# Kernel optimization log

Measured on AMD Instinct MI355X. Metric: run time of the kernel, lower is better.

## Reference

```python
import jax, jax.numpy as jnp
import numpy as np

N, E = 50000, 800000
H, C_HID = 4, 64  # heads, hidden_units
C_IN, C_OUT = 256, 64
NEG_SLOPE = 0.2
EPS = 1e-16


def gat_conv(x, src, dst, W, att_src, att_dst, bias):
    """PyG GATConv with concat=False (mean over heads) + bias.
    x: [N, F_in], W: [F_in, H*C], att_*: [H, C], bias: [C]."""
    n = x.shape[0]
    h = (x @ W).reshape(n, H, -1)                     # [N, H, C]
    a_src = jnp.sum(h * att_src, axis=-1)             # [N, H]
    a_dst = jnp.sum(h * att_dst, axis=-1)             # [N, H]
    e = jax.nn.leaky_relu(a_src[src] + a_dst[dst], NEG_SLOPE)  # [E, H]
    # segment softmax grouped by destination node
    m = jax.ops.segment_max(e, dst, num_segments=n)   # [N, H]
    e = jnp.exp(e - m[dst])
    denom = jax.ops.segment_sum(e, dst, num_segments=n)
    alpha = e / (denom[dst] + EPS)                    # [E, H]
    msg = h[src] * alpha[:, :, None]                  # [E, H, C]
    out = jax.ops.segment_sum(msg, dst, num_segments=n)  # [N, H, C]
    return out.mean(axis=1) + bias                    # concat=False -> head mean


def setup_inputs() -> dict:
    key = jax.random.key(0)
    ks = jax.random.split(key, 16)
    inp = {
        "x": jax.random.normal(ks[0], (N, C_IN), dtype=jnp.float32),
        "edge_index": jax.random.randint(ks[1], (2, E), 0, N, dtype=jnp.int64),
    }
    dims = [(C_IN, C_HID), (C_HID, C_HID), (C_HID, C_OUT)]
    for i, (fi, fo) in enumerate(dims, start=1):
        inp[f"W{i}"] = jax.random.normal(ks[2 + 4 * (i - 1)], (fi, H * fo), dtype=jnp.float32) * (1.0 / np.sqrt(fi))
        inp[f"as{i}"] = jax.random.normal(ks[3 + 4 * (i - 1)], (H, fo), dtype=jnp.float32) * 0.1
        inp[f"ad{i}"] = jax.random.normal(ks[4 + 4 * (i - 1)], (H, fo), dtype=jnp.float32) * 0.1
        inp[f"b{i}"] = jnp.zeros((fo,), dtype=jnp.float32)
    return inp


def reference(x, edge_index, W1, as1, ad1, b1, W2, as2, ad2, b2, W3, as3, ad3, b3):
    n = x.shape[0]
    loop = jnp.arange(n, dtype=edge_index.dtype)
    src = jnp.concatenate([edge_index[0], loop])  # add_self_loops=True (PyG default)
    dst = jnp.concatenate([edge_index[1], loop])
    layers = [(W1, as1, ad1, b1), (W2, as2, ad2, b2), (W3, as3, ad3, b3)]
    for (W, a_s, a_d, b) in layers:
        x = gat_conv(x, src, dst, W, a_s, a_d, b)
        x = jax.nn.relu(x)  # dropout is identity at inference
    return jax.nn.log_softmax(x, axis=-1)
```

## Files before the change

### kernel.cpp

```cpp
#include <hip/hip_runtime.h>
#include <hip/hip_bf16.h>
#include <math.h>
#include <stdint.h>

#define HEADS 4
#define CH 64
#define HC 256
#define NEG 0.2f
#define EPSV 1e-16f
#define NEGBIG -3.0e38f

typedef __attribute__((ext_vector_type(8))) short short8;
typedef __attribute__((ext_vector_type(4))) float f32x4;
typedef _Float16 f16_t;
typedef __fp16 fp16x2 __attribute__((ext_vector_type(2)));

__device__ __forceinline__ float lrelu(float x) { return x > 0.f ? x : NEG * x; }

__device__ __forceinline__ unsigned short f2bf(float f) {
  __hip_bfloat16 b = __float2bfloat16(f);
  return *reinterpret_cast<unsigned short*>(&b);
}
__device__ __forceinline__ unsigned short f16b(float f) {
  return __builtin_bit_cast(unsigned short, (f16_t)f);
}
__device__ __forceinline__ float dot2acc(unsigned int a, unsigned int h, float acc) {
#if __has_builtin(__builtin_amdgcn_fdot2)
  return __builtin_amdgcn_fdot2(__builtin_bit_cast(fp16x2, a),
                                __builtin_bit_cast(fp16x2, h), acc, false);
#else
  fp16x2 av = __builtin_bit_cast(fp16x2, a);
  fp16x2 hv = __builtin_bit_cast(fp16x2, h);
  return acc + (float)av[0] * (float)hv[0] + (float)av[1] * (float)hv[1];
#endif
}

__global__ __launch_bounds__(256) void wprep_k(const float* __restrict__ W,
                                               unsigned short* __restrict__ Wt,
                                               int K) {
  int i = blockIdx.x * 256 + threadIdx.x;
  if (i >= K * 256) return;
  int k = i >> 8, n = i & 255;
  Wt[(size_t)n * K + k] = f2bf(W[i]);
}

__global__ __launch_bounds__(256) void mfma_gat_k(const float* __restrict__ Af,
                                                  const unsigned short* __restrict__ Ab,
                                                  const unsigned short* __restrict__ Wt,
                                                  const float* __restrict__ att_s,
                                                  const float* __restrict__ att_d,
                                                  unsigned short* __restrict__ ht16,
                                                  float* __restrict__ a_src,
                                                  float* __restrict__ a_dst,
                                                  int M, int K, int a_is_f32) {
  __shared__ unsigned short As[32 * 40];
  __shared__ unsigned short Bs[256 * 40];
  __shared__ unsigned short Cs[32 * 258];

  int tid = threadIdx.x;
  int bm = blockIdx.x * 32;
  int w = tid >> 6, l = tid & 63;
  int lr = l & 15, lk = l >> 4;
  int row_s = tid >> 3, seg = tid & 7;

  f32x4 acc[2][4];
  #pragma unroll
  for (int rt = 0; rt < 2; ++rt)
    #pragma unroll
    for (int ct = 0; ct < 4; ++ct) {
      f32x4 z = {0.f, 0.f, 0.f, 0.f};
      acc[rt][ct] = z;
    }

  for (int k0 = 0; k0 < K; k0 += 32) {
    if (a_is_f32) {
      float4 v = make_float4(0.f, 0.f, 0.f, 0.f);
      if (bm + row_s < M)
        v = *reinterpret_cast<const float4*>(Af + (size_t)(bm + row_s) * K + k0 + seg * 4);
      ushort4 u;
      u.x = f2bf(v.x); u.y = f2bf(v.y); u.z = f2bf(v.z); u.w = f2bf(v.w);
      *reinterpret_cast<ushort4*>(&As[row_s * 40 + seg * 4]) = u;
    } else {
      ushort4 u = make_ushort4(0, 0, 0, 0);
      if (bm + row_s < M)
        u = *reinterpret_cast<const ushort4*>(Ab + (size_t)(bm + row_s) * K + k0 + seg * 4);
      *reinterpret_cast<ushort4*>(&As[row_s * 40 + seg * 4]) = u;
    }
    {
      const uint4* srcq = reinterpret_cast<const uint4*>(Wt + (size_t)tid * K + k0);
      uint4 q0 = srcq[0], q1 = srcq[1], q2 = srcq[2], q3 = srcq[3];
      uint4* dstq = reinterpret_cast<uint4*>(&Bs[tid * 40]);
      dstq[0] = q0; dstq[1] = q1; dstq[2] = q2; dstq[3] = q3;
    }
    __syncthreads();
    short8 bfr[4];
    #pragma unroll
    for (int ct = 0; ct < 4; ++ct)
      bfr[ct] = *reinterpret_cast<const short8*>(&Bs[(w * 64 + ct * 16 + lr) * 40 + lk * 8]);
    #pragma unroll
    for (int rt = 0; rt < 2; ++rt) {
      short8 af = *reinterpret_cast<const short8*>(&As[(rt * 16 + lr) * 40 + lk * 8]);
      #pragma unroll
      for (int ct = 0; ct < 4; ++ct)
        acc[rt][ct] = __builtin_amdgcn_mfma_f32_16x16x32_bf16(af, bfr[ct], acc[rt][ct], 0, 0, 0);
    }
    __syncthreads();
  }

  #pragma unroll
  for (int rt = 0; rt < 2; ++rt)
    #pragma unroll
    for (int ct = 0; ct < 4; ++ct)
      #pragma unroll
      for (int r = 0; r < 4; ++r) {
        int row = rt * 16 + lk * 4 + r;
        int c = ct * 16 + lr;
        Cs[row * 258 + c * 4 + w] = f16b(acc[rt][ct][r]);
      }
  __syncthreads();

  if (bm + row_s < M) {
    ushort4* dst = reinterpret_cast<ushort4*>(ht16 + (size_t)(bm + row_s) * HC + seg * 32);
    const unsigned short* srcp = &Cs[row_s * 258 + seg * 32];
    #pragma unroll
    for (int q = 0; q < 4; ++q)
      dst[q] = *reinterpret_cast<const ushort4*>(srcp + q * 4);
  }

  {
    int nd = tid >> 3, q = tid & 7, h = q >> 1, half = q & 1;
    float ps = 0.f, pd = 0.f;
    const float* ats = att_s + h * 64 + half * 32;
    const float* atd = att_d + h * 64 + half * 32;
    const unsigned short* cp = &Cs[nd * 258 + (half * 32) * 4 + h];
    #pragma unroll
    for (int c = 0; c < 32; ++c) {
      float hv = (float)__builtin_bit_cast(f16_t, cp[c * 4]);
      ps += hv * ats[c];
      pd += hv * atd[c];
    }
    ps += __shfl_xor(ps, 1);
    pd += __shfl_xor(pd, 1);
    if (!(q & 1) && bm + nd < M) {
      a_src[(size_t)(bm + nd) * 4 + h] = ps;
      a_dst[(size_t)(bm + nd) * 4 + h] = pd;
    }
  }
}

__global__ __launch_bounds__(256) void zero2_k(int* __restrict__ a, int* __restrict__ b, int n) {
  int i = blockIdx.x * blockDim.x + threadIdx.x;
  if (i < n) { a[i] = 0; b[i] = 0; }
}

__global__ __launch_bounds__(256) void hist_k(const int* __restrict__ dst, int* __restrict__ count, int E) {
  int e = blockIdx.x * blockDim.x + threadIdx.x;
  if (e < E) atomicAdd(&count[dst[e]], 1);
}

__global__ __launch_bounds__(512) void scan1_k(const int* __restrict__ count,
                                               int* __restrict__ rp,
                                               int* __restrict__ bsum, int n) {
  __shared__ int sh[512];
  int tx = threadIdx.x;
  int i = blockIdx.x * 512 + tx;
  int v = (i < n) ? count[i] : 0;
  sh[tx] = v;
  __syncthreads();
  #pragma unroll
  for (int off = 1; off < 512; off <<= 1) {
    int t = (tx >= off) ? sh[tx - off] : 0;
    __syncthreads();
    sh[tx] += t;
    __syncthreads();
  }
  if (i < n) rp[i] = sh[tx] - v;
  if (tx == 511) bsum[blockIdx.x] = sh[511];
}

__global__ __launch_bounds__(128) void scan2_k(int* __restrict__ bsum, int nb) {
  __shared__ int sh[128];
  int tx = threadIdx.x;
  int v = (tx < nb) ? bsum[tx] : 0;
  sh[tx] = v;
  __syncthreads();
  #pragma unroll
  for (int off = 1; off < 128; off <<= 1) {
    int t = (tx >= off) ? sh[tx - off] : 0;
    __syncthreads();
    sh[tx] += t;
    __syncthreads();
  }
  if (tx < nb) bsum[tx] = sh[tx] - v;
}

__global__ __launch_bounds__(512) void scan3_k(int* __restrict__ rp, const int* __restrict__ bsum,
                                               int n, int E) {
  int i = blockIdx.x * 512 + threadIdx.x;
  if (i < n) rp[i] += bsum[blockIdx.x];
  if (i == 0) rp[n] = E;
}

__global__ __launch_bounds__(256) void scatter_k(const int* __restrict__ src, const int* __restrict__ dst,
                                                 const int* __restrict__ rp, int* __restrict__ cursor,
                                                 int* __restrict__ csr_src, int E) {
  int e = blockIdx.x * blockDim.x + threadIdx.x;
  if (e >= E) return;
  int d = dst[e];
  int pos = rp[d] + atomicAdd(&cursor[d], 1);
  csr_src[pos] = src[e];
}

__global__ __launch_bounds__(256) void soft_agg_k(const int* __restrict__ rp,
                                                  const int* __restrict__ csr_src,
                                                  const float* __restrict__ a_src,
                                                  const float* __restrict__ a_dst,
                                                  const unsigned short* __restrict__ ht16,
                                                  const float* __restrict__ bias,
                                                  float* __restrict__ outf,
                                                  unsigned short* __restrict__ outb,
                                                  int N, int do_lsm) {
  __shared__ uint4 rec[4][17];
  int tid  = threadIdx.x;
  int w    = tid >> 6;
  int lane = tid & 63;
  int wid  = (blockIdx.x * blockDim.x + tid) >> 6;
  if (wid >= N) return;
  int rs = rp[wid], re = rp[wid + 1];
  int ep = lane & 15;
  int h  = lane >> 4;

  float adh = a_dst[(size_t)wid * 4 + h];
  float ash = a_src[(size_t)wid * 4 + h];
  float es  = lrelu(ash + adh);

  int s0 = 0, s1 = 0;
  float e0 = NEGBIG, e1 = NEGBIG;
  if (rs + ep < re) {
    s0 = csr_src[rs + ep];
    e0 = lrelu(a_src[(size_t)s0 * 4 + h] + adh);
  }
  if (rs + 16 + ep < re) {
    s1 = csr_src[rs + 16 + ep];
    e1 = lrelu(a_src[(size_t)s1 * 4 + h] + adh);
  }
  float m = fmaxf(es, fmaxf(e0, e1));
  for (int base = rs + 32; base < re; base += 16) {
    if (base + ep < re) {
      int s = csr_src[base + ep];
      m = fmaxf(m, lrelu(a_src[(size_t)s * 4 + h] + adh));
    }
  }
  #pragma unroll
  for (int off = 8; off > 0; off >>= 1) m = fmaxf(m, __shfl_xor(m, off));

  float p0 = expf(e0 - m), p1 = expf(e1 - m);
  float dn = p0 + p1;
  for (int base = rs + 32; base < re; base += 16) {
    if (base + ep < re) {
      int s = csr_src[base + ep];
      dn += expf(lrelu(a_src[(size_t)s * 4 + h] + adh) - m);
    }
  }
  #pragma unroll
  for (int off = 8; off > 0; off >>= 1) dn += __shfl_xor(dn, off);
  float sp = expf(es - m);
  dn += sp;
  float rr = 1.f / (dn + EPSV);

  unsigned short* recb = reinterpret_cast<unsigned short*>(&rec[w][0]);
  float acc = 0.f;
  const unsigned short* hl = ht16 + lane * 4;

  auto agg = [&](int cnt) {
    int k = 0;
    for (; k + 4 <= cnt; k += 4) {
      uint4 r0 = rec[w][k + 0], r1 = rec[w][k + 1];
      uint4 r2 = rec[w][k + 2], r3 = rec[w][k + 3];
      int t0 = __builtin_amdgcn_readfirstlane((int)r0.z);
      int t1 = __builtin_amdgcn_readfirstlane((int)r1.z);
      int t2 = __builtin_amdgcn_readfirstlane((int)r2.z);
      int t3 = __builtin_amdgcn_readfirstlane((int)r3.z);
      uint2 h0 = *reinterpret_cast<const uint2*>(hl + (size_t)t0 * HC);
      uint2 h1 = *reinterpret_cast<const uint2*>(hl + (size_t)t1 * HC);
      uint2 h2 = *reinterpret_cast<const uint2*>(hl + (size_t)t2 * HC);
      uint2 h3 = *reinterpret_cast<const uint2*>(hl + (size_t)t3 * HC);
      acc = dot2acc(r0.x, h0.x, acc); acc = dot2acc(r0.y, h0.y, acc);
      acc = dot2acc(r1.x, h1.x, acc); acc = dot2acc(r1.y, h1.y, acc);
      acc = dot2acc(r2.x, h2.x, acc); acc = dot2acc(r2.y, h2.y, acc);
      acc = dot2acc(r3.x, h3.x, acc); acc = dot2acc(r3.y, h3.y, acc);
    }
    for (; k < cnt; ++k) {
      uint4 r0 = rec[w][k];
      int t0 = __builtin_amdgcn_readfirstlane((int)r0.z);
      uint2 hv = *reinterpret_cast<const uint2*>(hl + (size_t)t0 * HC);
      acc = dot2acc(r0.x, hv.x, acc);
      acc = dot2acc(r0.y, hv.y, acc);
    }
  };

  if (ep == 0) recb[16 * 8 + h] = f16b(sp * rr);
  recb[ep * 8 + h] = f16b(p0 * rr);
  if (h == 0) *reinterpret_cast<int*>(recb + ep * 8 + 4) = s0;
  {
    int cnt = re - rs; if (cnt > 16) cnt = 16;
    agg(cnt);
  }
  if (re > rs + 16) {
    recb[ep * 8 + h] = f16b(p1 * rr);
    if (h == 0) *reinterpret_cast<int*>(recb + ep * 8 + 4) = s1;
    int cnt = re - rs - 16; if (cnt > 16) cnt = 16;
    agg(cnt);
  }
  for (int base = rs + 32; base < re; base += 16) {
    int s = 0;
    float e = NEGBIG;
    if (base + ep < re) {
      s = csr_src[base + ep];
      e = lrelu(a_src[(size_t)s * 4 + h] + adh);
    }
    recb[ep * 8 + h] = f16b(expf(e - m) * rr);
    if (h == 0) *reinterpret_cast<int*>(recb + ep * 8 + 4) = s;
    int cnt = re - base; if (cnt > 16) cnt = 16;
    agg(cnt);
  }

  uint2 sa = *reinterpret_cast<const uint2*>(&rec[w][16]);
  uint2 shv = *reinterpret_cast<const uint2*>(ht16 + (size_t)wid * HC + lane * 4);
  acc = dot2acc(sa.x, shv.x, acc);
  acc = dot2acc(sa.y, shv.y, acc);
  float v = acc * 0.25f + bias[lane];
  v = fmaxf(v, 0.f);
  if (do_lsm) {
    float mx = v;
    #pragma unroll
    for (int off = 32; off > 0; off >>= 1) mx = fmaxf(mx, __shfl_xor(mx, off));
    float ex = expf(v - mx);
    float sm = ex;
    #pragma unroll
    for (int off = 32; off > 0; off >>= 1) sm += __shfl_xor(sm, off);
    outf[(size_t)wid * CH + lane] = v - mx - logf(sm);
  } else {
    outb[(size_t)wid * CH + lane] = f2bf(v);
  }
}

extern "C" void kernel_launch(void* const* d_in, const int* in_sizes, int n_in,
                              void* d_out, int out_size, void* d_ws, size_t ws_size,
                              hipStream_t stream) {
  const float* x0 = (const float*)d_in[0];
  const int*   ei = (const int*)d_in[1];
  int N = in_sizes[0] / HC;
  int E = in_sizes[1] / 2;
  const int* srcp = ei;
  const int* dstp = ei + E;

  const float* W[3]  = {(const float*)d_in[2], (const float*)d_in[6],  (const float*)d_in[10]};
  const float* AS[3] = {(const float*)d_in[3], (const float*)d_in[7],  (const float*)d_in[11]};
  const float* AD[3] = {(const float*)d_in[4], (const float*)d_in[8],  (const float*)d_in[12]};
  const float* BI[3] = {(const float*)d_in[5], (const float*)d_in[9],  (const float*)d_in[13]};
  int Kdim[3] = {256, 64, 64};

  char* ws = (char*)d_ws;
  size_t off = 0;
  auto alloc = [&](size_t bytes) {
    void* p = ws + off;
    off += (bytes + 255) & ~(size_t)255;
    return p;
  };
  unsigned short* ht16    = (unsigned short*)alloc((size_t)N * HC * 2);
  unsigned short* xb16    = (unsigned short*)alloc((size_t)N * CH * 2);
  float*          a_s     = (float*)alloc((size_t)N * 4 * 4);
  float*          a_d     = (float*)alloc((size_t)N * 4 * 4);
  int*            rowp    = (int*)alloc((size_t)(N + 1) * 4);
  int*            cursor  = (int*)alloc((size_t)N * 4);
  int*            csr_src = (int*)alloc((size_t)E * 4);
  int*            bsum    = (int*)alloc(512 * 4);
  unsigned short* Wt[3];
  Wt[0] = (unsigned short*)alloc((size_t)256 * 256 * 2);
  Wt[1] = (unsigned short*)alloc((size_t)256 * 64 * 2);
  Wt[2] = (unsigned short*)alloc((size_t)256 * 64 * 2);

  for (int L = 0; L < 3; ++L) {
    int tot = Kdim[L] * 256;
    wprep_k<<<(tot + 255) / 256, 256, 0, stream>>>(W[L], Wt[L], Kdim[L]);
  }

  int nb = (N + 511) / 512;
  zero2_k<<<(N + 255) / 256, 256, 0, stream>>>(cursor, rowp, N);
  hist_k<<<(E + 255) / 256, 256, 0, stream>>>(dstp, rowp, E);
  scan1_k<<<nb, 512, 0, stream>>>(rowp, rowp, bsum, N);
  scan2_k<<<1, 128, 0, stream>>>(bsum, nb);
  scan3_k<<<nb, 512, 0, stream>>>(rowp, bsum, N, E);
  scatter_k<<<(E + 255) / 256, 256, 0, stream>>>(srcp, dstp, rowp, cursor, csr_src, E);

  for (int L = 0; L < 3; ++L) {
    int K = Kdim[L];
    mfma_gat_k<<<(N + 31) / 32, 256, 0, stream>>>(
        (L == 0) ? x0 : nullptr, (L == 0) ? nullptr : xb16,
        Wt[L], AS[L], AD[L], ht16, a_s, a_d, N, K, (L == 0) ? 1 : 0);
    soft_agg_k<<<(N + 3) / 4, 256, 0, stream>>>(rowp, csr_src, a_s, a_d, ht16, BI[L],
                                                (float*)d_out, xb16, N, (L == 2) ? 1 : 0);
  }
}
```

Measured before the change: 383.9 us.

## Merge weight-prep launches, load B fragments directly, unroll aggregation by 8

Fuses the three per-layer weight transpose/convert launches into one kernel and replaces the zeroing kernel with two hipMemsetAsync calls, cutting launch overhead. The MFMA GEMM no longer stages the weight tile through shared memory. Each wave now reads its B fragments straight from global memory, which removes one LDS copy and one barrier per k-step but relies on cache hits for reuse. The aggregation loop gains an 8-edge unrolled path to keep more gather loads in flight, at some cost in register use.

```diff
diff --git a/kernel.cpp b/kernel.cpp
--- a/kernel.cpp
+++ b/kernel.cpp
@@ -35,13 +35,23 @@
 #endif
 }
 
-__global__ __launch_bounds__(256) void wprep_k(const float* __restrict__ W,
-                                               unsigned short* __restrict__ Wt,
-                                               int K) {
+__global__ __launch_bounds__(256) void wprep3_k(const float* __restrict__ W0,
+                                                const float* __restrict__ W1,
+                                                const float* __restrict__ W2,
+                                                unsigned short* __restrict__ T0,
+                                                unsigned short* __restrict__ T1,
+                                                unsigned short* __restrict__ T2) {
   int i = blockIdx.x * 256 + threadIdx.x;
-  if (i >= K * 256) return;
-  int k = i >> 8, n = i & 255;
-  Wt[(size_t)n * K + k] = f2bf(W[i]);
+  if (i < 65536) {
+    int k = i >> 8, n = i & 255;
+    T0[n * 256 + k] = f2bf(W0[i]);
+  } else if (i < 81920) {
+    int j = i - 65536, k = j >> 8, n = j & 255;
+    T1[n * 64 + k] = f2bf(W1[j]);
+  } else if (i < 98304) {
+    int j = i - 81920, k = j >> 8, n = j & 255;
+    T2[n * 64 + k] = f2bf(W2[j]);
+  }
 }
 
 __global__ __launch_bounds__(256) void mfma_gat_k(const float* __restrict__ Af,
@@ -54,7 +64,6 @@
                                                   float* __restrict__ a_dst,
                                                   int M, int K, int a_is_f32) {
   __shared__ unsigned short As[32 * 40];
-  __shared__ unsigned short Bs[256 * 40];
   __shared__ unsigned short Cs[32 * 258];
 
   int tid = threadIdx.x;
@@ -71,6 +80,8 @@
       f32x4 z = {0.f, 0.f, 0.f, 0.f};
       acc[rt][ct] = z;
     }
+
+  const unsigned short* wp0 = Wt + (size_t)(w * 64 + lr) * K + lk * 8;
 
   for (int k0 = 0; k0 < K; k0 += 32) {
     if (a_is_f32) {
@@ -86,17 +97,11 @@
         u = *reinterpret_cast<const ushort4*>(Ab + (size_t)(bm + row_s) * K + k0 + seg * 4);
       *reinterpret_cast<ushort4*>(&As[row_s * 40 + seg * 4]) = u;
     }
-    {
-      const uint4* srcq = reinterpret_cast<const uint4*>(Wt + (size_t)tid * K + k0);
-      uint4 q0 = srcq[0], q1 = srcq[1], q2 = srcq[2], q3 = srcq[3];
-      uint4* dstq = reinterpret_cast<uint4*>(&Bs[tid * 40]);
-      dstq[0] = q0; dstq[1] = q1; dstq[2] = q2; dstq[3] = q3;
-    }
-    __syncthreads();
     short8 bfr[4];
     #pragma unroll
     for (int ct = 0; ct < 4; ++ct)
-      bfr[ct] = *reinterpret_cast<const short8*>(&Bs[(w * 64 + ct * 16 + lr) * 40 + lk * 8]);
+      bfr[ct] = *reinterpret_cast<const short8*>(wp0 + (size_t)ct * 16 * K + k0);
+    __syncthreads();
     #pragma unroll
     for (int rt = 0; rt < 2; ++rt) {
       short8 af = *reinterpret_cast<const short8*>(&As[(rt * 16 + lr) * 40 + lk * 8]);
@@ -146,11 +151,6 @@
       a_dst[(size_t)(bm + nd) * 4 + h] = pd;
     }
   }
-}
-
-__global__ __launch_bounds__(256) void zero2_k(int* __restrict__ a, int* __restrict__ b, int n) {
-  int i = blockIdx.x * blockDim.x + threadIdx.x;
-  if (i < n) { a[i] = 0; b[i] = 0; }
 }
 
 __global__ __launch_bounds__(256) void hist_k(const int* __restrict__ dst, int* __restrict__ count, int E) {
@@ -274,6 +274,36 @@
 
   auto agg = [&](int cnt) {
     int k = 0;
+    for (; k + 8 <= cnt; k += 8) {
+      uint4 r0 = rec[w][k + 0], r1 = rec[w][k + 1];
+      uint4 r2 = rec[w][k + 2], r3 = rec[w][k + 3];
+      uint4 r4 = rec[w][k + 4], r5 = rec[w][k + 5];
+      uint4 r6 = rec[w][k + 6], r7 = rec[w][k + 7];
+      int t0 = __builtin_amdgcn_readfirstlane((int)r0.z);
+      int t1 = __builtin_amdgcn_readfirstlane((int)r1.z);
+      int t2 = __builtin_amdgcn_readfirstlane((int)r2.z);
+      int t3 = __builtin_amdgcn_readfirstlane((int)r3.z);
+      int t4 = __builtin_amdgcn_readfirstlane((int)r4.z);
+      int t5 = __builtin_amdgcn_readfirstlane((int)r5.z);
+      int t6 = __builtin_amdgcn_readfirstlane((int)r6.z);
+      int t7 = __builtin_amdgcn_readfirstlane((int)r7.z);
+      uint2 h0 = *reinterpret_cast<const uint2*>(hl + (size_t)t0 * HC);
+      uint2 h1 = *reinterpret_cast<const uint2*>(hl + (size_t)t1 * HC);
+      uint2 h2 = *reinterpret_cast<const uint2*>(hl + (size_t)t2 * HC);
+      uint2 h3 = *reinterpret_cast<const uint2*>(hl + (size_t)t3 * HC);
+      uint2 h4 = *reinterpret_cast<const uint2*>(hl + (size_t)t4 * HC);
+      uint2 h5 = *reinterpret_cast<const uint2*>(hl + (size_t)t5 * HC);
+      uint2 h6 = *reinterpret_cast<const uint2*>(hl + (size_t)t6 * HC);
+      uint2 h7 = *reinterpret_cast<const uint2*>(hl + (size_t)t7 * HC);
+      acc = dot2acc(r0.x, h0.x, acc); acc = dot2acc(r0.y, h0.y, acc);
+      acc = dot2acc(r1.x, h1.x, acc); acc = dot2acc(r1.y, h1.y, acc);
+      acc = dot2acc(r2.x, h2.x, acc); acc = dot2acc(r2.y, h2.y, acc);
+      acc = dot2acc(r3.x, h3.x, acc); acc = dot2acc(r3.y, h3.y, acc);
+      acc = dot2acc(r4.x, h4.x, acc); acc = dot2acc(r4.y, h4.y, acc);
+      acc = dot2acc(r5.x, h5.x, acc); acc = dot2acc(r5.y, h5.y, acc);
+      acc = dot2acc(r6.x, h6.x, acc); acc = dot2acc(r6.y, h6.y, acc);
+      acc = dot2acc(r7.x, h7.x, acc); acc = dot2acc(r7.y, h7.y, acc);
+    }
     for (; k + 4 <= cnt; k += 4) {
       uint4 r0 = rec[w][k + 0], r1 = rec[w][k + 1];
       uint4 r2 = rec[w][k + 2], r3 = rec[w][k + 3];
@@ -381,13 +411,11 @@
   Wt[1] = (unsigned short*)alloc((size_t)256 * 64 * 2);
   Wt[2] = (unsigned short*)alloc((size_t)256 * 64 * 2);
 
-  for (int L = 0; L < 3; ++L) {
-    int tot = Kdim[L] * 256;
-    wprep_k<<<(tot + 255) / 256, 256, 0, stream>>>(W[L], Wt[L], Kdim[L]);
-  }
+  wprep3_k<<<384, 256, 0, stream>>>(W[0], W[1], W[2], Wt[0], Wt[1], Wt[2]);
 
   int nb = (N + 511) / 512;
-  zero2_k<<<(N + 255) / 256, 256, 0, stream>>>(cursor, rowp, N);
+  hipMemsetAsync(cursor, 0, (size_t)N * 4, stream);
+  hipMemsetAsync(rowp, 0, (size_t)N * 4, stream);
   hist_k<<<(E + 255) / 256, 256, 0, stream>>>(dstp, rowp, E);
   scan1_k<<<nb, 512, 0, stream>>>(rowp, rowp, bsum, N);
   scan2_k<<<1, 128, 0, stream>>>(bsum, nb);
```

Measured after the change: 384.8 us (median of 2 runs). Within noise of the previous version (+0.3%).
